# Kernel tuning notes

Hardware: AMD Instinct MI355X
Metric: run time of the kernel (lower is better)

Reference implementation:

```python
import jax, jax.numpy as jnp
import numpy as np

EPSILON = 1e-8
PSD_EPS = 1e-5


def _mask_norm(mask):
    # torch.norm(mask, inf, dim=1, keepdim=True): max |.| over F axis
    max_abs = jnp.max(jnp.abs(mask), axis=1, keepdims=True)
    return mask / (max_abs + EPSILON)


def _estimate_psd(mask, cm):
    # mask: [B,F,T] real; cm: [B,C,F,T] complex -> psd [B,F,C,C]
    x = jnp.transpose(cm, (0, 2, 1, 3))            # [B,F,C,T]
    m = mask[:, :, None, :]                        # [B,F,1,T]
    nom = jnp.einsum('bfct,bfdt->bfcd', x * m, jnp.conj(x))
    den = jnp.clip(jnp.sum(m, axis=-1, keepdims=True), PSD_EPS, None)
    psd = nom / den
    return psd + 1j * jnp.asarray(PSD_EPS, psd.real.dtype)


def setup_inputs() -> dict:
    key = jax.random.key(0)
    k1, k2, k3, k4 = jax.random.split(key, 4)
    B, C, F, T = 8, 8, 257, 1500
    return {
        'speech_mask': jax.random.uniform(k1, (B, F, T), dtype=jnp.float32),
        'noise_mask': jax.random.uniform(k2, (B, F, T), dtype=jnp.float32),
        'cm_real': jax.random.normal(k3, (B, C, F, T), dtype=jnp.float32),
        'cm_imag': jax.random.normal(k4, (B, C, F, T), dtype=jnp.float32),
    }


def reference(speech_mask, noise_mask, cm_real, cm_imag):
    eps = EPSILON
    cm = cm_real + 1j * cm_imag                    # [B,C,F,T] complex64
    B, C, F, T = cm.shape

    sm = _mask_norm(speech_mask)
    nm = _mask_norm(noise_mask)

    speech_psd = _estimate_psd(sm, cm) + 1j * jnp.float32(eps)   # [B,F,C,C]
    noise_psd = _estimate_psd(nm, cm) + 1j * jnp.float32(eps)

    # diagonal loading + inverse, stabilized
    eye = jnp.eye(C, dtype=noise_psd.dtype)
    noise_psd_inv = jnp.linalg.inv(noise_psd + eye * eps)
    noise_psd_inv = noise_psd_inv + 1j * jnp.float32(eps)

    A = noise_psd_inv @ speech_psd                 # [B,F,C,C]
    tr = jnp.einsum('bfcc->bf', A) + eps           # trace [B,F]

    ref_vec = jnp.zeros((B, C), dtype=A.dtype).at[:, 0].set(1.0)
    u = jnp.einsum('bfcd,bd->bfc', A, ref_vec)     # [B,F,C]
    weight = u / tr[..., None]                     # [B,F,C]
    w = jnp.transpose(weight, (0, 2, 1))           # [B,C,F]

    # apply beamformer: sum_c conj(w) * cm -> [B,F,T]
    out = jnp.einsum('bcf,bcft->bft', jnp.conj(w), cm)
    return jnp.stack([out.real, out.imag])         # [2,B,F,T] float32
```

## Files before the change

### kernel.cpp

```cpp
#include <hip/hip_runtime.h>

#define Bb 8
#define Cc 8
#define Ff 257
#define Tt 1500
#define P2 750
#define P4 375
#define BF (Bb*Ff)

__device__ __forceinline__ constexpr int odIdx(int c, int d) { return 7*c - c*(c-1)/2 + (d-c-1); }

constexpr float EPSv   = 1e-8f;
constexpr float PSDEPS = 1e-5f;
constexpr float IMADD  = 1e-5f + 1e-8f;

__device__ __forceinline__ void gl2lds16(const float* g, float* l) {
    __builtin_amdgcn_global_load_lds((const __attribute__((address_space(1))) void*)g,
                                     (__attribute__((address_space(3))) void*)l, 16, 0, 0);
}

__global__ void mask_pmax(const float* __restrict__ sm, const float* __restrict__ nm,
                          float* __restrict__ pmax_s, float* __restrict__ pmax_n) {
    int t  = blockIdx.x * 256 + threadIdx.x;
    int ch = blockIdx.y;
    int b  = blockIdx.z;
    if (t >= Tt) return;
    int f0 = ch * 33, f1 = min(Ff, f0 + 33);
    float ms = 0.f, mn = 0.f;
    for (int f = f0; f < f1; ++f) {
        ms = fmaxf(ms, fabsf(sm[(b*Ff + f)*Tt + t]));
        mn = fmaxf(mn, fabsf(nm[(b*Ff + f)*Tt + t]));
    }
    pmax_s[(b*8 + ch)*Tt + t] = ms;
    pmax_n[(b*8 + ch)*Tt + t] = mn;
}

__global__ void mask_inv(const float* __restrict__ pmax_s, const float* __restrict__ pmax_n,
                         float* __restrict__ inv_s, float* __restrict__ inv_n) {
    int t = blockIdx.x * 256 + threadIdx.x;
    int b = blockIdx.y;
    if (t >= Tt) return;
    float ms = 0.f, mn = 0.f;
    #pragma unroll
    for (int ch = 0; ch < 8; ++ch) {
        ms = fmaxf(ms, pmax_s[(b*8 + ch)*Tt + t]);
        mn = fmaxf(mn, pmax_n[(b*8 + ch)*Tt + t]);
    }
    inv_s[b*Tt + t] = 1.0f / (ms + EPSv);
    inv_n[b*Tt + t] = 1.0f / (mn + EPSv);
}

__global__ __launch_bounds__(256) __attribute__((amdgpu_waves_per_eu(4, 4)))
void mvdr_main(
    const float* __restrict__ smask, const float* __restrict__ nmask,
    const float* __restrict__ cmr,   const float* __restrict__ cmi,
    const float* __restrict__ inv_s, const float* __restrict__ inv_n,
    float* __restrict__ out)
{
    const int blk = blockIdx.x;
    const int b = blk / Ff, f = blk % Ff;
    const int tid  = threadIdx.x;
    const int wid  = tid >> 6;
    const int lane = tid & 63;
    const int msel = __builtin_amdgcn_readfirstlane(wid >> 1);
    const int part = __builtin_amdgcn_readfirstlane(wid & 1);

    __shared__ float tile0[20*128];
    __shared__ float tile1[20*128];

    auto segbase = [&](int s) -> const float* {
        if (s < 8)   return cmr + ((size_t)(b*Cc + s)      *Ff + f)*Tt;
        if (s < 16)  return cmi + ((size_t)(b*Cc + (s-8))  *Ff + f)*Tt;
        if (s == 16) return smask + ((size_t)b*Ff + f)*Tt;
        if (s == 17) return nmask + ((size_t)b*Ff + f)*Tt;
        if (s == 18) return inv_s + (size_t)b*Tt;
        return inv_n + (size_t)b*Tt;
    };
    auto pick = [&](int j) -> const float* {
        const float* e = segbase(2*j);
        const float* o = segbase(2*j + 1);
        return (lane & 32) ? o : e;
    };
    const float* Pa  = pick(wid);
    const float* Pb  = pick(wid + 4);
    const bool  has3 = (wid < 2);
    const float* Pc  = has3 ? pick(wid + 8) : Pa;

    auto stage = [&](int it, float* dst) {
        int fi = it*128 + ((lane & 31) << 2);
        fi = min(fi, Tt - 4);
        gl2lds16(Pa + fi, dst + (2*wid)*128);
        gl2lds16(Pb + fi, dst + (2*(wid+4))*128);
        if (has3) gl2lds16(Pc + fi, dst + (2*(wid+8))*128);
    };

    float acc[32];
    #pragma unroll
    for (int v = 0; v < 32; ++v) acc[v] = 0.f;
    float summ = 0.f;

    auto computeIter = [&](int it, const float* cur) {
        const float2* c2 = (const float2*)cur;
        float2 mk = c2[(16 + msel)*64 + lane];
        float2 iv = c2[(18 + msel)*64 + lane];
        float2 xr[8], xi[8];
        #pragma unroll
        for (int c = 0; c < 8; ++c) { xr[c] = c2[c*64 + lane]; xi[c] = c2[(8+c)*64 + lane]; }
        const float valid = (lane + it*64 < P2) ? 1.0f : 0.0f;
        float mx = mk.x * iv.x * valid, my = mk.y * iv.y * valid;
        if (part == 0) {
            summ += mx + my;
            #pragma unroll
            for (int c = 0; c < 8; ++c) {
                float ax = mx*xr[c].x, ay = my*xr[c].y, bx = mx*xi[c].x, by = my*xi[c].y;
                if (c < 4) {
                    float t0 = acc[28 + c];
                    t0 = fmaf(ax, xr[c].x, t0); t0 = fmaf(bx, xi[c].x, t0);
                    t0 = fmaf(ay, xr[c].y, t0); t0 = fmaf(by, xi[c].y, t0);
                    acc[28 + c] = t0;
                }
                #pragma unroll
                for (int d = c + 1; d < 8; ++d) {
                    const int k = odIdx(c, d);
                    float t0 = acc[k];
                    t0 = fmaf(ax, xr[d].x, t0); t0 = fmaf(bx, xi[d].x, t0);
                    t0 = fmaf(ay, xr[d].y, t0); t0 = fmaf(by, xi[d].y, t0);
                    acc[k] = t0;
                }
            }
        } else {
            #pragma unroll
            for (int c = 0; c < 8; ++c) {
                float ax = mx*xr[c].x, ay = my*xr[c].y, bx = mx*xi[c].x, by = my*xi[c].y;
                if (c >= 4) {
                    float t0 = acc[28 + (c - 4)];
                    t0 = fmaf(ax, xr[c].x, t0); t0 = fmaf(bx, xi[c].x, t0);
                    t0 = fmaf(ay, xr[c].y, t0); t0 = fmaf(by, xi[c].y, t0);
                    acc[28 + (c - 4)] = t0;
                }
                #pragma unroll
                for (int d = c + 1; d < 8; ++d) {
                    const int j = odIdx(c, d);
                    float t1 = acc[j];
                    t1 = fmaf(bx, xr[d].x, t1); t1 = fmaf(-ax, xi[d].x, t1);
                    t1 = fmaf(by, xr[d].y, t1); t1 = fmaf(-ay, xi[d].y, t1);
                    acc[j] = t1;
                }
            }
        }
    };

    stage(0, tile0);
    __syncthreads();
    #pragma unroll 1
    for (int it = 0; it < 12; it += 2) {
        stage(it + 1, tile1);
        computeIter(it, tile0);
        __syncthreads();
        if (it < 10) stage(it + 2, tile0);
        computeIter(it + 1, tile1);
        __syncthreads();
    }

    __shared__ float OffRe[2][28], OffIm[2][28], Diagm[2][8];
    __shared__ float sumSN[2];

    #pragma unroll
    for (int o = 1; o <= 32; o <<= 1) {
        if (part == 0) summ += __shfl_xor(summ, o, 64);
        #pragma unroll
        for (int v = 0; v < 32; ++v) acc[v] += __shfl_xor(acc[v], o, 64);
    }
    if (lane == 0) {
        if (part == 0) {
            #pragma unroll
            for (int v = 0; v < 28; ++v) OffRe[msel][v] = acc[v];
            #pragma unroll
            for (int v = 0; v < 4; ++v) Diagm[msel][v] = acc[28 + v];
            sumSN[msel] = summ;
        } else {
            #pragma unroll
            for (int v = 0; v < 28; ++v) OffIm[msel][v] = acc[v];
            #pragma unroll
            for (int v = 0; v < 4; ++v) Diagm[msel][4 + v] = acc[28 + v];
        }
    }
    __syncthreads();

    __shared__ float SreM[64], SimM[64];
    __shared__ float Are[128], Aim[128];
    __shared__ float dre[8], dim_[8], wre[8], wim[8];

    if (tid < 64) {
        const float den_s = fmaxf(sumSN[0], PSDEPS);
        const float den_n = fmaxf(sumSN[1], PSDEPS);
        int cc_, dd_;
        float sv, nv;
        if (tid < 36) {
            int k = tid, c = 0; while (k >= 8 - c) { k -= 8 - c; ++c; } cc_ = c; dd_ = c + k;
            if (cc_ == dd_) { sv = Diagm[0][cc_] / den_s; nv = Diagm[1][cc_] / den_n; }
            else { int o = odIdx(cc_, dd_); sv = OffRe[0][o] / den_s; nv = OffRe[1][o] / den_n; }
        } else {
            int k = tid - 36, c = 0; while (k >= 7 - c) { k -= 7 - c; ++c; } cc_ = c; dd_ = c + k + 1;
            sv = OffIm[0][tid - 36] / den_s; nv = OffIm[1][tid - 36] / den_n;
        }
        if (tid < 36) {
            SreM[cc_*8 + dd_] = sv; SreM[dd_*8 + cc_] = sv;
            float nvd = nv + (cc_ == dd_ ? EPSv : 0.f);
            Are[cc_*16 + dd_] = nvd; Are[dd_*16 + cc_] = nvd;
            if (cc_ == dd_) { SimM[cc_*8 + cc_] = IMADD; Aim[cc_*16 + cc_] = IMADD; }
        } else {
            SimM[cc_*8 + dd_] = IMADD + sv; SimM[dd_*8 + cc_] = IMADD - sv;
            Aim[cc_*16 + dd_] = IMADD + nv; Aim[dd_*16 + cc_] = IMADD - nv;
        }
        int r = tid >> 3, j = tid & 7;
        Are[r*16 + 8 + j] = (r == j) ? 1.f : 0.f;
        Aim[r*16 + 8 + j] = 0.f;
    }
    __syncthreads();

    {
        const bool act = tid < 64;
        const int r = (tid >> 3) & 7, cA = tid & 7;
        for (int k = 0; k < 8; ++k) {
            float pr = Are[k*16 + k], pi = Aim[k*16 + k];
            float idn = 1.0f / (pr*pr + pi*pi);
            float ipr = pr*idn, ipi = -pi*idn;
            if (act && r == k) {
                float ar0 = Are[k*16 + cA],     ai0 = Aim[k*16 + cA];
                Are[k*16 + cA]     = ar0*ipr - ai0*ipi; Aim[k*16 + cA]     = ar0*ipi + ai0*ipr;
                float ar1 = Are[k*16 + cA + 8], ai1 = Aim[k*16 + cA + 8];
                Are[k*16 + cA + 8] = ar1*ipr - ai1*ipi; Aim[k*16 + cA + 8] = ar1*ipi + ai1*ipr;
            }
            __syncthreads();
            float fr = Are[r*16 + k], fi = Aim[r*16 + k];
            float p0r = Are[k*16 + cA],     p0i = Aim[k*16 + cA];
            float p1r = Are[k*16 + cA + 8], p1i = Aim[k*16 + cA + 8];
            float o0r = 0.f, o0i = 0.f, o1r = 0.f, o1i = 0.f;
            if (r != k) {
                o0r = Are[r*16 + cA]     - (fr*p0r - fi*p0i);
                o0i = Aim[r*16 + cA]     - (fr*p0i + fi*p0r);
                o1r = Are[r*16 + cA + 8] - (fr*p1r - fi*p1i);
                o1i = Aim[r*16 + cA + 8] - (fr*p1i + fi*p1r);
            }
            __syncthreads();
            if (act && r != k) {
                Are[r*16 + cA]     = o0r; Aim[r*16 + cA]     = o0i;
                Are[r*16 + cA + 8] = o1r; Aim[r*16 + cA + 8] = o1i;
            }
            __syncthreads();
        }
    }

    if (tid < 8) {
        int c = tid;
        float ur = 0.f, ui = 0.f, tr_r = 0.f, tr_i = 0.f;
        #pragma unroll
        for (int j = 0; j < 8; ++j) {
            float vr = Are[c*16 + 8 + j], vi = Aim[c*16 + 8 + j] + EPSv;
            float s0r = SreM[j*8 + 0], s0i = SimM[j*8 + 0];
            ur += vr*s0r - vi*s0i; ui += vr*s0i + vi*s0r;
            float scr = SreM[j*8 + c], sci = SimM[j*8 + c];
            tr_r += vr*scr - vi*sci; tr_i += vr*sci + vi*scr;
        }
        dre[c] = tr_r; dim_[c] = tr_i;
        wre[c] = ur;   wim[c]  = ui;
    }
    __syncthreads();
    if (tid < 8) {
        float tr_r = EPSv, tr_i = 0.f;
        #pragma unroll
        for (int j = 0; j < 8; ++j) { tr_r += dre[j]; tr_i += dim_[j]; }
        float idn = 1.0f / (tr_r*tr_r + tr_i*tr_i);
        float ur = wre[tid], ui = wim[tid];
        wre[tid] = (ur*tr_r + ui*tr_i) * idn;
        wim[tid] = (ui*tr_r - ur*tr_i) * idn;
    }
    __syncthreads();

    float wr[8], wi[8];
    #pragma unroll
    for (int c = 0; c < 8; ++c) { wr[c] = wre[c]; wi[c] = wim[c]; }

    const int cstride4 = Ff * P4;
    const float4* xr4 = (const float4*)(cmr + ((size_t)(b*Cc)*Ff + f)*Tt);
    const float4* xi4 = (const float4*)(cmi + ((size_t)(b*Cc)*Ff + f)*Tt);
    float4* outr4 = (float4*)out + (b*Ff + f)*P4;
    float4* outi4 = (float4*)out + (Bb*Ff)*P4 + (b*Ff + f)*P4;
    for (int pp = tid; pp < P4; pp += 256) {
        float rx = 0.f, ry = 0.f, rz = 0.f, rw = 0.f;
        float ix = 0.f, iy = 0.f, iz = 0.f, iw = 0.f;
        #pragma unroll
        for (int c = 0; c < 8; ++c) {
            float4 a  = xr4[pp + c*cstride4];
            float4 bb = xi4[pp + c*cstride4];
            rx = fmaf(wr[c], a.x, fmaf(wi[c], bb.x, rx));
            ry = fmaf(wr[c], a.y, fmaf(wi[c], bb.y, ry));
            rz = fmaf(wr[c], a.z, fmaf(wi[c], bb.z, rz));
            rw = fmaf(wr[c], a.w, fmaf(wi[c], bb.w, rw));
            ix = fmaf(wr[c], bb.x, fmaf(-wi[c], a.x, ix));
            iy = fmaf(wr[c], bb.y, fmaf(-wi[c], a.y, iy));
            iz = fmaf(wr[c], bb.z, fmaf(-wi[c], a.z, iz));
            iw = fmaf(wr[c], bb.w, fmaf(-wi[c], a.w, iw));
        }
        outr4[pp] = make_float4(rx, ry, rz, rw);
        outi4[pp] = make_float4(ix, iy, iz, iw);
    }
}

extern "C" void kernel_launch(void* const* d_in, const int* in_sizes, int n_in,
                              void* d_out, int out_size, void* d_ws, size_t ws_size,
                              hipStream_t stream) {
    const float* smask = (const float*)d_in[0];
    const float* nmask = (const float*)d_in[1];
    const float* cmr   = (const float*)d_in[2];
    const float* cmi   = (const float*)d_in[3];
    float* ws = (float*)d_ws;
    float* pmax_s = ws;
    float* pmax_n = ws + 96000;
    float* inv_s  = ws + 192000;
    float* inv_n  = ws + 204000;

    mask_pmax<<<dim3(6, 8, 8), 256, 0, stream>>>(smask, nmask, pmax_s, pmax_n);
    mask_inv <<<dim3(6, 8),    256, 0, stream>>>(pmax_s, pmax_n, inv_s, inv_n);
    mvdr_main<<<BF, 256, 0, stream>>>(smask, nmask, cmr, cmi, inv_s, inv_n, (float*)d_out);
}
```

Before: 373.4 us.

## Split PSD accumulation across eight waves with 4x4 channel quadrants

```diff
diff --git a/kernel.cpp b/kernel.cpp
--- a/kernel.cpp
+++ b/kernel.cpp
@@ -8,7 +8,7 @@
 #define P4 375
 #define BF (Bb*Ff)
 
-__device__ __forceinline__ constexpr int odIdx(int c, int d) { return 7*c - c*(c-1)/2 + (d-c-1); }
+__device__ __forceinline__ constexpr int idx4(int c, int d) { return c*(7-c)/2 + d - c - 1; }
 
 constexpr float EPSv   = 1e-8f;
 constexpr float PSDEPS = 1e-5f;
@@ -50,7 +50,7 @@
     inv_n[b*Tt + t] = 1.0f / (mn + EPSv);
 }
 
-__global__ __launch_bounds__(256) __attribute__((amdgpu_waves_per_eu(4, 4)))
+__global__ __launch_bounds__(512)
 void mvdr_main(
     const float* __restrict__ smask, const float* __restrict__ nmask,
     const float* __restrict__ cmr,   const float* __restrict__ cmi,
@@ -62,8 +62,8 @@
     const int tid  = threadIdx.x;
     const int wid  = tid >> 6;
     const int lane = tid & 63;
-    const int msel = __builtin_amdgcn_readfirstlane(wid >> 1);
-    const int part = __builtin_amdgcn_readfirstlane(wid & 1);
+    const int msel = __builtin_amdgcn_readfirstlane(wid >> 2);
+    const int quad = __builtin_amdgcn_readfirstlane(wid & 3);
 
     __shared__ float tile0[20*128];
     __shared__ float tile1[20*128];
@@ -81,70 +81,85 @@
         const float* o = segbase(2*j + 1);
         return (lane & 32) ? o : e;
     };
-    const float* Pa  = pick(wid);
-    const float* Pb  = pick(wid + 4);
-    const bool  has3 = (wid < 2);
-    const float* Pc  = has3 ? pick(wid + 8) : Pa;
+    const float* Pa   = pick(wid);
+    const bool  has2  = (wid < 2);
+    const float* Pb   = has2 ? pick(wid + 8) : Pa;
 
     auto stage = [&](int it, float* dst) {
         int fi = it*128 + ((lane & 31) << 2);
         fi = min(fi, Tt - 4);
-        gl2lds16(Pa + fi, dst + (2*wid)*128);
-        gl2lds16(Pb + fi, dst + (2*(wid+4))*128);
-        if (has3) gl2lds16(Pc + fi, dst + (2*(wid+8))*128);
+        gl2lds16(Pa + fi, dst + wid*256);
+        if (has2) gl2lds16(Pb + fi, dst + (wid + 8)*256);
     };
 
-    float acc[32];
+    float acc[16];
     #pragma unroll
-    for (int v = 0; v < 32; ++v) acc[v] = 0.f;
+    for (int v = 0; v < 16; ++v) acc[v] = 0.f;
     float summ = 0.f;
 
     auto computeIter = [&](int it, const float* cur) {
         const float2* c2 = (const float2*)cur;
         float2 mk = c2[(16 + msel)*64 + lane];
         float2 iv = c2[(18 + msel)*64 + lane];
-        float2 xr[8], xi[8];
-        #pragma unroll
-        for (int c = 0; c < 8; ++c) { xr[c] = c2[c*64 + lane]; xi[c] = c2[(8+c)*64 + lane]; }
         const float valid = (lane + it*64 < P2) ? 1.0f : 0.0f;
-        float mx = mk.x * iv.x * valid, my = mk.y * iv.y * valid;
-        if (part == 0) {
-            summ += mx + my;
+        const float mx = mk.x * iv.x * valid, my = mk.y * iv.y * valid;
+
+        if (quad <= 1) {
+            const int c0 = quad * 4;
+            float2 xr[4], xi[4];
             #pragma unroll
-            for (int c = 0; c < 8; ++c) {
+            for (int j = 0; j < 4; ++j) {
+                xr[j] = c2[(c0 + j)*64 + lane];
+                xi[j] = c2[(8 + c0 + j)*64 + lane];
+            }
+            if (quad == 0) summ += mx + my;
+            #pragma unroll
+            for (int c = 0; c < 4; ++c) {
                 float ax = mx*xr[c].x, ay = my*xr[c].y, bx = mx*xi[c].x, by = my*xi[c].y;
-                if (c < 4) {
-                    float t0 = acc[28 + c];
+                {
+                    float t0 = acc[c];
                     t0 = fmaf(ax, xr[c].x, t0); t0 = fmaf(bx, xi[c].x, t0);
                     t0 = fmaf(ay, xr[c].y, t0); t0 = fmaf(by, xi[c].y, t0);
-                    acc[28 + c] = t0;
+                    acc[c] = t0;
                 }
                 #pragma unroll
-                for (int d = c + 1; d < 8; ++d) {
-                    const int k = odIdx(c, d);
-                    float t0 = acc[k];
+                for (int d = c + 1; d < 4; ++d) {
+                    const int p = idx4(c, d);
+                    float t0 = acc[4 + 2*p], t1 = acc[5 + 2*p];
                     t0 = fmaf(ax, xr[d].x, t0); t0 = fmaf(bx, xi[d].x, t0);
                     t0 = fmaf(ay, xr[d].y, t0); t0 = fmaf(by, xi[d].y, t0);
-                    acc[k] = t0;
-                }
-            }
-        } else {
-            #pragma unroll
-            for (int c = 0; c < 8; ++c) {
-                float ax = mx*xr[c].x, ay = my*xr[c].y, bx = mx*xi[c].x, by = my*xi[c].y;
-                if (c >= 4) {
-                    float t0 = acc[28 + (c - 4)];
-                    t0 = fmaf(ax, xr[c].x, t0); t0 = fmaf(bx, xi[c].x, t0);
-                    t0 = fmaf(ay, xr[c].y, t0); t0 = fmaf(by, xi[c].y, t0);
-                    acc[28 + (c - 4)] = t0;
-                }
-                #pragma unroll
-                for (int d = c + 1; d < 8; ++d) {
-                    const int j = odIdx(c, d);
-                    float t1 = acc[j];
                     t1 = fmaf(bx, xr[d].x, t1); t1 = fmaf(-ax, xi[d].x, t1);
                     t1 = fmaf(by, xr[d].y, t1); t1 = fmaf(-ay, xi[d].y, t1);
-                    acc[j] = t1;
+                    acc[4 + 2*p] = t0; acc[5 + 2*p] = t1;
+                }
+            }
+        } else {
+            float2 xrh[4], xih[4];
+            #pragma unroll
+            for (int j = 0; j < 4; ++j) {
+                xrh[j] = c2[(4 + j)*64 + lane];
+                xih[j] = c2[(12 + j)*64 + lane];
+            }
+            #pragma unroll
+            for (int c = 0; c < 4; ++c) {
+                float2 xrc = c2[c*64 + lane], xic = c2[(8 + c)*64 + lane];
+                float ax = mx*xrc.x, ay = my*xrc.y, bx = mx*xic.x, by = my*xic.y;
+                if (quad == 2) {
+                    #pragma unroll
+                    for (int d = 0; d < 4; ++d) {
+                        float t0 = acc[c*4 + d];
+                        t0 = fmaf(ax, xrh[d].x, t0); t0 = fmaf(bx, xih[d].x, t0);
+                        t0 = fmaf(ay, xrh[d].y, t0); t0 = fmaf(by, xih[d].y, t0);
+                        acc[c*4 + d] = t0;
+                    }
+                } else {
+                    #pragma unroll
+                    for (int d = 0; d < 4; ++d) {
+                        float t1 = acc[c*4 + d];
+                        t1 = fmaf(bx, xrh[d].x, t1); t1 = fmaf(-ax, xih[d].x, t1);
+                        t1 = fmaf(by, xrh[d].y, t1); t1 = fmaf(-ay, xih[d].y, t1);
+                        acc[c*4 + d] = t1;
+                    }
                 }
             }
         }
@@ -162,28 +177,19 @@
         __syncthreads();
     }
 
-    __shared__ float OffRe[2][28], OffIm[2][28], Diagm[2][8];
+    __shared__ float Racc[8][16];
     __shared__ float sumSN[2];
 
     #pragma unroll
     for (int o = 1; o <= 32; o <<= 1) {
-        if (part == 0) summ += __shfl_xor(summ, o, 64);
-        #pragma unroll
-        for (int v = 0; v < 32; ++v) acc[v] += __shfl_xor(acc[v], o, 64);
+        if (quad == 0) summ += __shfl_xor(summ, o, 64);
+        #pragma unroll
+        for (int v = 0; v < 16; ++v) acc[v] += __shfl_xor(acc[v], o, 64);
     }
     if (lane == 0) {
-        if (part == 0) {
-            #pragma unroll
-            for (int v = 0; v < 28; ++v) OffRe[msel][v] = acc[v];
-            #pragma unroll
-            for (int v = 0; v < 4; ++v) Diagm[msel][v] = acc[28 + v];
-            sumSN[msel] = summ;
-        } else {
-            #pragma unroll
-            for (int v = 0; v < 28; ++v) OffIm[msel][v] = acc[v];
-            #pragma unroll
-            for (int v = 0; v < 4; ++v) Diagm[msel][4 + v] = acc[28 + v];
-        }
+        #pragma unroll
+        for (int v = 0; v < 16; ++v) Racc[wid][v] = acc[v];
+        if (quad == 0) sumSN[msel] = summ;
     }
     __syncthreads();
 
@@ -194,16 +200,20 @@
     if (tid < 64) {
         const float den_s = fmaxf(sumSN[0], PSDEPS);
         const float den_n = fmaxf(sumSN[1], PSDEPS);
-        int cc_, dd_;
-        float sv, nv;
+        int cc_, dd_, part;
         if (tid < 36) {
             int k = tid, c = 0; while (k >= 8 - c) { k -= 8 - c; ++c; } cc_ = c; dd_ = c + k;
-            if (cc_ == dd_) { sv = Diagm[0][cc_] / den_s; nv = Diagm[1][cc_] / den_n; }
-            else { int o = odIdx(cc_, dd_); sv = OffRe[0][o] / den_s; nv = OffRe[1][o] / den_n; }
+            part = 0;
         } else {
             int k = tid - 36, c = 0; while (k >= 7 - c) { k -= 7 - c; ++c; } cc_ = c; dd_ = c + k + 1;
-            sv = OffIm[0][tid - 36] / den_s; nv = OffIm[1][tid - 36] / den_n;
-        }
+            part = 1;
+        }
+        int widx, idx;
+        if (dd_ < 4)       { widx = 0; idx = (cc_ == dd_) ? cc_ : 4 + 2*idx4(cc_, dd_) + part; }
+        else if (cc_ >= 4) { widx = 1; idx = (cc_ == dd_) ? cc_ - 4 : 4 + 2*idx4(cc_-4, dd_-4) + part; }
+        else               { widx = 2 + part; idx = cc_*4 + (dd_ - 4); }
+        float sv = Racc[widx][idx]     / den_s;
+        float nv = Racc[4 + widx][idx] / den_n;
         if (tid < 36) {
             SreM[cc_*8 + dd_] = sv; SreM[dd_*8 + cc_] = sv;
             float nvd = nv + (cc_ == dd_ ? EPSv : 0.f);
@@ -287,7 +297,7 @@
     const float4* xi4 = (const float4*)(cmi + ((size_t)(b*Cc)*Ff + f)*Tt);
     float4* outr4 = (float4*)out + (b*Ff + f)*P4;
     float4* outi4 = (float4*)out + (Bb*Ff)*P4 + (b*Ff + f)*P4;
-    for (int pp = tid; pp < P4; pp += 256) {
+    for (int pp = tid; pp < P4; pp += 512) {
         float rx = 0.f, ry = 0.f, rz = 0.f, rw = 0.f;
         float ix = 0.f, iy = 0.f, iz = 0.f, iw = 0.f;
         #pragma unroll
@@ -323,5 +333,5 @@
 
     mask_pmax<<<dim3(6, 8, 8), 256, 0, stream>>>(smask, nmask, pmax_s, pmax_n);
     mask_inv <<<dim3(6, 8),    256, 0, stream>>>(pmax_s, pmax_n, inv_s, inv_n);
-    mvdr_main<<<BF, 256, 0, stream>>>(smask, nmask, cmr, cmi, inv_s, inv_n, (float*)d_out);
-}
+    mvdr_main<<<BF, 512, 0, stream>>>(smask, nmask, cmr, cmi, inv_s, inv_n, (float*)d_out);
+}
```

Result: faster. 301.7 us (-19.2%).
